# Kernel optimization log

Hardware: AMD Instinct MI355X
Metric: run time of the kernel (lower is better)

## Reference

```python
import jax, jax.numpy as jnp
import numpy as np

ALPHA = 1.0
GAMMA = 2.0
SMOOTH = 1e-07
B, S = 8192, 4096


def setup_inputs() -> dict:
    key = jax.random.key(0)
    k1, k2, k3, k4 = jax.random.split(key, 4)
    scores = jax.random.normal(k1, (B, S), dtype=jnp.float32)
    head_position = jax.random.randint(k2, (B,), 0, S, dtype=jnp.int64) if jax.config.jax_enable_x64 else jax.random.randint(k2, (B,), 0, S).astype(jnp.int32)
    tail_position = jax.random.randint(k3, (B,), 0, S).astype(head_position.dtype)
    score_mask = jax.random.randint(k4, (B, S), 0, 2, dtype=jnp.int32)
    return {"scores": scores, "head_position": head_position,
            "tail_position": tail_position, "score_mask": score_mask}


def reference(scores, head_position, tail_position, score_mask):
    # scores: [B, S] float; head/tail_position: [B] int; score_mask: [B, S] int
    batch_size = scores.shape[0]
    bidx = jnp.arange(batch_size)
    # exclude head and tail positions from the negative set
    m = score_mask.at[bidx, head_position].set(-1)
    m = m.at[bidx, tail_position].set(-1)
    neg = (m == 1)  # [B, S] candidate negatives
    # positive score per sample, broadcast against all candidates
    pos = jnp.take_along_axis(scores, tail_position[:, None], axis=1)  # [B, 1]
    # log_softmax over the pair [pos, neg_j] at index 0 == -softplus(neg - pos)
    logpt = -jax.nn.softplus(scores - pos)  # [B, S]
    pt = jnp.clip(jnp.exp(logpt), SMOOTH, 1.0 - SMOOTH)
    fl = -ALPHA * jnp.power(1.0 - pt, GAMMA) * logpt  # [B, S] per-pair focal loss
    negf = neg.astype(scores.dtype)
    cnt = negf.sum(axis=1)  # [B] number of negatives
    # per-sample focal_loss is the MEAN over its pairs; samples with 0 negs skipped
    per_sample = jnp.where(cnt > 0, (fl * negf).sum(axis=1) / jnp.maximum(cnt, 1.0), 0.0)
    return per_sample.sum() / batch_size
```

## Files before the change

### kernel.cpp

```cpp
#include <hip/hip_runtime.h>


#define GLL(gaddr, laddr)                                                          \
    __builtin_amdgcn_global_load_lds(                                              \
        (const __attribute__((address_space(1))) void*)(gaddr),                    \
        (__attribute__((address_space(3))) void*)(laddr), 16, 0, 0)

__device__ __forceinline__ float focal_term(float x) {
    const float e  = __expf(x);
    const float t  = 1.f + e;
    const float sp = __logf(t);
    const float pt = __builtin_amdgcn_rcpf(t);
    const float om = 1.f - pt;
    return om * om * sp;
}

template <int S>
__global__ __launch_bounds__(256, 8) void focal_row_kernel(
    const float* __restrict__ scores,
    const int*   __restrict__ head_pos,
    const int*   __restrict__ tail_pos,
    const int*   __restrict__ mask,
    float*       __restrict__ row_out,
    int B)
{
    constexpr int NIT = S / 256;
    static_assert(S % 256 == 0 && NIT >= 4, "shape");

    __shared__ float s_lds[4][2][256];
    __shared__ int   m_lds[4][2][256];

    const int lane = threadIdx.x & 63;
    const int wid  = threadIdx.x >> 6;
    const int row  = blockIdx.x * 4 + wid;
    if (row >= B) return;

    const int head = head_pos[row];
    const int tail = tail_pos[row];
    const float* srow = scores + (size_t)row * S;
    const int*   mrow = mask   + (size_t)row * S;
    const float pos = srow[tail];

    asm volatile("s_waitcnt vmcnt(0) lgkmcnt(0)" ::: "memory");

    GLL(srow + lane * 4,       &s_lds[wid][0][0]);
    GLL(mrow + lane * 4,       &m_lds[wid][0][0]);
    GLL(srow + 256 + lane * 4, &s_lds[wid][1][0]);
    GLL(mrow + 256 + lane * 4, &m_lds[wid][1][0]);

    float fsum = 0.f, cnt = 0.f;

    #pragma unroll
    for (int i = 0; i < NIT; ++i) {
        if (i == NIT - 1) asm volatile("s_waitcnt vmcnt(0)" ::: "memory");
        else              asm volatile("s_waitcnt vmcnt(2)" ::: "memory");
        const float4 sv = reinterpret_cast<const float4*>(&s_lds[wid][i & 1][0])[lane];
        const int4   mv = reinterpret_cast<const int4*>(&m_lds[wid][i & 1][0])[lane];
        asm volatile("s_waitcnt lgkmcnt(0)" ::: "memory");
        __builtin_amdgcn_sched_barrier(0);
        if (i + 2 < NIT) {
            GLL(srow + (i + 2) * 256 + lane * 4, &s_lds[wid][i & 1][0]);
            GLL(mrow + (i + 2) * 256 + lane * 4, &m_lds[wid][i & 1][0]);
        }
        const float se[4] = {sv.x, sv.y, sv.z, sv.w};
        const int   me[4] = {mv.x, mv.y, mv.z, mv.w};
        #pragma unroll
        for (int k = 0; k < 4; ++k) {
            const float fl = focal_term(se[k] - pos);
            const float on = (float)me[k];
            fsum = fmaf(fl, on, fsum);
            cnt += on;
        }
    }

    #pragma unroll
    for (int off = 32; off; off >>= 1) {
        fsum += __shfl_down(fsum, off, 64);
        cnt  += __shfl_down(cnt,  off, 64);
    }

    if (lane == 0) {
        if (mrow[head] == 1) { fsum -= focal_term(srow[head] - pos); cnt -= 1.f; }
        if (tail != head && mrow[tail] == 1) { fsum -= focal_term(0.f); cnt -= 1.f; }
        row_out[row] = (cnt > 0.f) ? fsum / cnt : 0.f;
    }
}

__global__ __launch_bounds__(256) void focal_row_generic(
    const float* __restrict__ scores,
    const int*   __restrict__ head_pos,
    const int*   __restrict__ tail_pos,
    const int*   __restrict__ mask,
    float*       __restrict__ row_out,
    int S)
{
    const int row  = blockIdx.x;
    const int tid  = threadIdx.x;
    const int head = head_pos[row];
    const int tail = tail_pos[row];
    const float* srow = scores + (size_t)row * S;
    const int*   mrow = mask   + (size_t)row * S;
    const float pos = srow[tail];
    float fsum = 0.f, cnt = 0.f;
    for (int idx = tid; idx < S; idx += 256) {
        const float fl = focal_term(srow[idx] - pos);
        if ((mrow[idx] == 1) && (idx != head) && (idx != tail)) { fsum += fl; cnt += 1.f; }
    }
    #pragma unroll
    for (int off = 32; off; off >>= 1) {
        fsum += __shfl_down(fsum, off, 64);
        cnt  += __shfl_down(cnt,  off, 64);
    }
    __shared__ float sf[4]; __shared__ float sc[4];
    const int wave = tid >> 6;
    if ((tid & 63) == 0) { sf[wave] = fsum; sc[wave] = cnt; }
    __syncthreads();
    if (tid == 0) {
        float tot = sf[0] + sf[1] + sf[2] + sf[3];
        float c   = sc[0] + sc[1] + sc[2] + sc[3];
        row_out[row] = (c > 0.f) ? tot / c : 0.f;
    }
}

__global__ __launch_bounds__(256) void final_reduce_kernel(
    const float* __restrict__ row_out, float* __restrict__ out, int B)
{
    float sum = 0.f;
    const float4* r4 = reinterpret_cast<const float4*>(row_out);
    const int nvec = B >> 2;
    for (int i = threadIdx.x; i < nvec; i += 256) {
        float4 v = r4[i];
        sum += (v.x + v.y) + (v.z + v.w);
    }
    #pragma unroll
    for (int off = 32; off; off >>= 1) sum += __shfl_down(sum, off, 64);
    __shared__ float sf[4];
    const int wave = threadIdx.x >> 6;
    if ((threadIdx.x & 63) == 0) sf[wave] = sum;
    __syncthreads();
    if (threadIdx.x == 0) out[0] = (sf[0] + sf[1] + sf[2] + sf[3]) / (float)B;
}

extern "C" void kernel_launch(void* const* d_in, const int* in_sizes, int n_in,
                              void* d_out, int out_size, void* d_ws, size_t ws_size,
                              hipStream_t stream)
{
    const float* scores = (const float*)d_in[0];
    const int*   headp  = (const int*)d_in[1];
    const int*   tailp  = (const int*)d_in[2];
    const int*   maskp  = (const int*)d_in[3];
    const int B = in_sizes[1];
    const int S = in_sizes[0] / B;

    float* rowbuf = (float*)d_ws;
    float* out    = (float*)d_out;

    if (S == 4096) {
        const int grid = (B + 3) / 4;
        focal_row_kernel<4096><<<grid, 256, 0, stream>>>(scores, headp, tailp, maskp, rowbuf, B);
    } else {
        focal_row_generic<<<B, 256, 0, stream>>>(scores, headp, tailp, maskp, rowbuf, S);
    }
    final_reduce_kernel<<<1, 256, 0, stream>>>(rowbuf, out, B);
}
```

Baseline: 283.7 us.

## Replace LDS double-buffered async loads with direct nontemporal vector register loads

Drops the global_load_lds double-buffering through shared memory, its manual waitcnt pipeline and the LDS allocation. Each lane now issues four 16-byte nontemporal loads of scores and mask per group straight into registers, then computes. This removes the LDS round trip and its occupancy cost. In exchange it depends on the compiler for latency hiding and may raise register pressure.

Result: faster. 260.0 us (-8.3%).

```diff
diff --git a/kernel.cpp b/kernel.cpp
--- a/kernel.cpp
+++ b/kernel.cpp
@@ -1,10 +1,8 @@
 #include <hip/hip_runtime.h>
 
 
-#define GLL(gaddr, laddr)                                                          \
-    __builtin_amdgcn_global_load_lds(                                              \
-        (const __attribute__((address_space(1))) void*)(gaddr),                    \
-        (__attribute__((address_space(3))) void*)(laddr), 16, 0, 0)
+using f32x4 = __attribute__((ext_vector_type(4))) float;
+using i32x4 = __attribute__((ext_vector_type(4))) int;
 
 __device__ __forceinline__ float focal_term(float x) {
     const float e  = __expf(x);
@@ -24,52 +22,40 @@
     float*       __restrict__ row_out,
     int B)
 {
-    constexpr int NIT = S / 256;
-    static_assert(S % 256 == 0 && NIT >= 4, "shape");
-
-    __shared__ float s_lds[4][2][256];
-    __shared__ int   m_lds[4][2][256];
-
     const int lane = threadIdx.x & 63;
-    const int wid  = threadIdx.x >> 6;
-    const int row  = blockIdx.x * 4 + wid;
+    const int row  = blockIdx.x * 4 + (threadIdx.x >> 6);
     if (row >= B) return;
 
     const int head = head_pos[row];
     const int tail = tail_pos[row];
     const float* srow = scores + (size_t)row * S;
     const int*   mrow = mask   + (size_t)row * S;
+    const f32x4* s4 = reinterpret_cast<const f32x4*>(srow);
+    const i32x4* m4 = reinterpret_cast<const i32x4*>(mrow);
     const float pos = srow[tail];
-
-    asm volatile("s_waitcnt vmcnt(0) lgkmcnt(0)" ::: "memory");
-
-    GLL(srow + lane * 4,       &s_lds[wid][0][0]);
-    GLL(mrow + lane * 4,       &m_lds[wid][0][0]);
-    GLL(srow + 256 + lane * 4, &s_lds[wid][1][0]);
-    GLL(mrow + 256 + lane * 4, &m_lds[wid][1][0]);
 
     float fsum = 0.f, cnt = 0.f;
 
+    constexpr int NV4 = S / 4 / 64;
+    static_assert(NV4 % 4 == 0, "S must be divisible by 1024");
     #pragma unroll
-    for (int i = 0; i < NIT; ++i) {
-        if (i == NIT - 1) asm volatile("s_waitcnt vmcnt(0)" ::: "memory");
-        else              asm volatile("s_waitcnt vmcnt(2)" ::: "memory");
-        const float4 sv = reinterpret_cast<const float4*>(&s_lds[wid][i & 1][0])[lane];
-        const int4   mv = reinterpret_cast<const int4*>(&m_lds[wid][i & 1][0])[lane];
-        asm volatile("s_waitcnt lgkmcnt(0)" ::: "memory");
-        __builtin_amdgcn_sched_barrier(0);
-        if (i + 2 < NIT) {
-            GLL(srow + (i + 2) * 256 + lane * 4, &s_lds[wid][i & 1][0]);
-            GLL(mrow + (i + 2) * 256 + lane * 4, &m_lds[wid][i & 1][0]);
+    for (int g = 0; g < NV4 / 4; ++g) {
+        f32x4 sv[4]; i32x4 mv[4];
+        #pragma unroll
+        for (int u = 0; u < 4; ++u) {
+            const int v = lane + 64 * (4 * g + u);
+            sv[u] = __builtin_nontemporal_load(&s4[v]);
+            mv[u] = __builtin_nontemporal_load(&m4[v]);
         }
-        const float se[4] = {sv.x, sv.y, sv.z, sv.w};
-        const int   me[4] = {mv.x, mv.y, mv.z, mv.w};
         #pragma unroll
-        for (int k = 0; k < 4; ++k) {
-            const float fl = focal_term(se[k] - pos);
-            const float on = (float)me[k];
-            fsum = fmaf(fl, on, fsum);
-            cnt += on;
+        for (int u = 0; u < 4; ++u) {
+            #pragma unroll
+            for (int k = 0; k < 4; ++k) {
+                const float fl = focal_term(sv[u][k] - pos);
+                const float on = (float)mv[u][k];
+                fsum = fmaf(fl, on, fsum);
+                cnt += on;
+            }
         }
     }
 
```
